# Kernel optimization log

Measured on AMD Instinct MI355X. Metric: run time of the kernel, lower is better.

The kernel has to match this reference:

```python
import jax, jax.numpy as jnp
import numpy as np

B, CIN, H, W = 8, 128, 32, 32
COUT, K, STRIDE, PAD = 128, 3, 1, 1
DK, DV, NH = 64, 64, 8
DKH, DVH = DK // NH, DV // NH


def conv2d(x, w, b, stride, pad):
    out = jax.lax.conv_general_dilated(
        x, w, (stride, stride), [(pad, pad), (pad, pad)],
        dimension_numbers=("NCHW", "OIHW", "NCHW"))
    return out + b[None, :, None, None]


def rel_to_abs(x):
    # x: (b, Nh, L, 2L-1) relative -> (b, Nh, L, L) absolute via pad/reshape/slice
    b, nh, L, _ = x.shape
    x = jnp.pad(x, ((0, 0), (0, 0), (0, 0), (0, 1)))          # (b,Nh,L,2L)
    flat = x.reshape(b, nh, L * 2 * L)
    flat = jnp.pad(flat, ((0, 0), (0, 0), (0, L - 1)))
    final = flat.reshape(b, nh, L + 1, 2 * L - 1)
    return final[:, :, :L, L - 1:]


def relative_logits_1d(q, key_rel, Hh, Ww, Nh, case):
    # q: (b, Nh, x, y, dkh); key_rel: (2*len-1, dkh)
    rel = jnp.einsum("bhxyd,md->bhxym", q, key_rel)
    rel = rel.reshape(-1, Nh * Hh, Ww, 2 * Ww - 1)
    rel = rel_to_abs(rel)
    rel = rel.reshape(-1, Nh, Hh, Ww, Ww)
    rel = jnp.tile(rel[:, :, :, None, :, :], (1, 1, 1, Hh, 1, 1))  # (b,Nh,H,H,W,W)
    if case == "h":
        # torch .transpose(2,4).transpose(3,5)
        rel = rel.transpose(0, 1, 4, 5, 2, 3)
    return rel.reshape(-1, Nh, Hh * Ww, Hh * Ww)


def reference(x, w_general, b_general, w_qkv, b_qkv, w_out, b_out, key_rel_h, key_rel_w):
    batch, _, height, width = x.shape
    conv_out = conv2d(x, w_general, b_general, STRIDE, PAD)

    qkv = conv2d(x, w_qkv, b_qkv, 1, 0)
    q, k, v = jnp.split(qkv, [DK, 2 * DK], axis=1)
    # split heads: (B, Nh, c//Nh, H, W)
    q = q.reshape(batch, NH, DKH, height, width)
    k = k.reshape(batch, NH, DKH, height, width)
    v = v.reshape(batch, NH, DVH, height, width)
    # faithful to original bug: q / dkh**(-0.5) == q * sqrt(dkh)
    q = q / (DKH ** (-0.5))

    flat_q = q.reshape(batch, NH, height * width, DKH)
    flat_k = k.reshape(batch, NH, height * width, DKH)
    flat_v = v.reshape(batch, NH, height * width, DVH)

    logits = jnp.einsum("bhnd,bhmd->bhnm", flat_q, flat_k)

    # relative position logits
    q5 = q.transpose(0, 1, 3, 4, 2)  # (B, Nh, H, W, dkh)
    logits = logits + relative_logits_1d(q5, key_rel_h, height, width, NH, "h")
    logits = logits + relative_logits_1d(q5.transpose(0, 1, 3, 2, 4), key_rel_w, height, width, NH, "w")

    weights = jax.nn.softmax(logits, axis=-1)
    attn = jnp.einsum("bhnm,bhmd->bhnd", weights, flat_v)
    attn = attn.reshape(batch, NH, height, width, DVH)
    # combine heads: (B, Nh*dvh, H, W)
    attn = attn.transpose(0, 1, 4, 2, 3).reshape(batch, NH * DVH, height, width)
    attn = conv2d(attn, w_out, b_out, STRIDE, PAD)
    return jnp.concatenate((conv_out, attn), axis=1)


def setup_inputs():
    key = jax.random.key(0)
    ks = jax.random.split(key, 8)
    f = jnp.float32
    x = jax.random.normal(ks[0], (B, CIN, H, W), f)
    w_general = jax.random.normal(ks[1], (COUT - DV, CIN, K, K), f) * 0.02
    b_general = jnp.zeros((COUT - DV,), f)
    w_qkv = jax.random.normal(ks[2], (2 * DK + DV, CIN, 1, 1), f) * 0.05
    b_qkv = jnp.zeros((2 * DK + DV,), f)
    w_out = jax.random.normal(ks[3], (DV, DV, K, K), f) * 0.05
    b_out = jnp.zeros((DV,), f)
    key_rel_h = jax.random.normal(ks[4], (2 * H - 1, DKH), f)
    key_rel_w = jax.random.normal(ks[5], (2 * W - 1, DKH), f)
    return {"x": x, "w_general": w_general, "b_general": b_general,
            "w_qkv": w_qkv, "b_qkv": b_qkv, "w_out": w_out, "b_out": b_out,
            "key_rel_h": key_rel_h, "key_rel_w": key_rel_w}
```

## Files before the change

### kernel.cpp

```cpp
#include <hip/hip_runtime.h>
#include <hip/hip_bf16.h>


#define NP 1024
#define QSCALE 2.8284271247461903f
#define LOG2E  1.4426950408889634f

using bf16 = __hip_bfloat16;
typedef unsigned short ushort;
typedef unsigned int uint;
using bf16x8 = __attribute__((ext_vector_type(8))) short;
using f32x4  = __attribute__((ext_vector_type(4))) float;
using f32x2  = __attribute__((ext_vector_type(2))) float;

__device__ __forceinline__ float b2f(bf16 v) { return __bfloat162float(v); }
__device__ __forceinline__ ushort f2b(float v) {
  bf16 h = __float2bfloat16(v);
  ushort u; __builtin_memcpy(&u, &h, 2); return u;
}
__device__ __forceinline__ f32x2 up2(uint u) {
  f32x2 r;
  r[0] = __uint_as_float(u << 16);
  r[1] = __uint_as_float(u & 0xffff0000u);
  return r;
}

__device__ __forceinline__ float dot8(const float* a, const float* b) {
  float s = a[0] * b[0];
  s = fmaf(a[1], b[1], s); s = fmaf(a[2], b[2], s); s = fmaf(a[3], b[3], s);
  s = fmaf(a[4], b[4], s); s = fmaf(a[5], b[5], s); s = fmaf(a[6], b[6], s);
  s = fmaf(a[7], b[7], s);
  return s;
}

__device__ __forceinline__ int fenc(float f) { int i = __float_as_int(f); return i < 0 ? (i ^ 0x7fffffff) : i; }
__device__ __forceinline__ float fdec(int i) { return __int_as_float(i < 0 ? (i ^ 0x7fffffff) : i); }

#if defined(__has_builtin)
#if __has_builtin(__builtin_amdgcn_exp2f)
#define EXP2F __builtin_amdgcn_exp2f
#else
#define EXP2F exp2f
#endif
#else
#define EXP2F exp2f
#endif

#define OFF_QBUF   0
#define OFF_KB16   524288
#define OFF_VTB    786432
#define OFF_XPB    1310720
#define OFF_APB    1902592
#define OFF_WGB    2198528
#define OFF_WOB    2235392
#define OFF_BG     2253824
#define OFF_BQKV   2253888
#define OFF_BO     2254080
#define OFF_KRH    2254144
#define OFF_KRW    2254648
#define OFF_FLAG   2255152

__global__ __launch_bounds__(256) void cvt_kernel(
    const void* __restrict__ p0, const void* __restrict__ p1, const void* __restrict__ p2,
    const void* __restrict__ p3, const void* __restrict__ p4, const void* __restrict__ p5,
    const void* __restrict__ p6, const void* __restrict__ p7, const void* __restrict__ p8,
    float* __restrict__ ws, int* __restrict__ flag)
{
  __shared__ int partial[4];
  __shared__ uint lds[64][65];
  int t = threadIdx.x;
  const unsigned* xraw = (const unsigned*)p0;
  int cnt = 0;
  for (int i = t; i < 1024; i += 256) {
    unsigned elo = (xraw[i] >> 7) & 0xffu;
    cnt += (elo >= 64u && elo <= 133u) ? 1 : 0;
  }
#pragma unroll
  for (int off = 1; off < 64; off <<= 1) cnt += __shfl_xor(cnt, off);
  if ((t & 63) == 0) partial[t >> 6] = cnt;
  __syncthreads();
  int tot = partial[0] + partial[1] + partial[2] + partial[3];
  int f32 = (tot >= 650) ? 0 : 1;
  if (blockIdx.x == 0 && t == 0) *flag = f32;

  int gsz = gridDim.x * 256;
  int gid = blockIdx.x * 256 + t;

  const void* src[5] = {p2, p4, p6, p7, p8};
  const int   n[5]    = {64, 192, 64, 504, 504};
  const int   doff[5] = {OFF_BG, OFF_BQKV, OFF_BO, OFF_KRH, OFF_KRW};
#pragma unroll
  for (int s = 0; s < 5; s++) {
    float* dst = ws + doff[s];
    if (f32) { const float* sp = (const float*)src[s];
      for (int i = gid; i < n[s]; i += gsz) dst[i] = sp[i];
    } else { const bf16* sp = (const bf16*)src[s];
      for (int i = gid; i < n[s]; i += gsz) dst[i] = b2f(sp[i]);
    }
  }

  {
    float4* z = (float4*)(ws + OFF_VTB);
    for (int i = gid; i < 131072; i += gsz) z[i] = float4{0.f, 0.f, 0.f, 0.f};
  }

  {
    uint4 z = {0u, 0u, 0u, 0u};
    uint4* xp = (uint4*)(ws + OFF_XPB);
    uint4* ap = (uint4*)(ws + OFF_APB);
    for (int s = gid; s < 9248; s += gsz) {
      int pb = s / 1156, rem = s - pb * 1156;
      int y = rem / 34, x = rem - y * 34;
      if (y == 0 || y == 33 || x == 0 || x == 33) {
        uint4* d1 = xp + (size_t)s * 16;
#pragma unroll
        for (int k = 0; k < 16; k++) d1[k] = z;
        uint4* d2 = ap + (size_t)s * 8;
#pragma unroll
        for (int k = 0; k < 8; k++) d2[k] = z;
      }
    }
  }

  {
    ushort* wgb = (ushort*)(ws + OFF_WGB);
    for (int s = gid; s < 73728; s += gsz) {
      int kykx = s >> 13, co = (s >> 7) & 63, ci = s & 127;
      int si = (co * 128 + ci) * 9 + kykx;
      wgb[s] = f32 ? f2b(((const float*)p1)[si]) : ((const ushort*)p1)[si];
    }
  }
  {
    ushort* wob = (ushort*)(ws + OFF_WOB);
    for (int s = gid; s < 36864; s += gsz) {
      int kykx = s >> 12, co = (s >> 6) & 63, ci = s & 63;
      int si = (co * 64 + ci) * 9 + kykx;
      wob[s] = f32 ? f2b(((const float*)p5)[si]) : ((const ushort*)p5)[si];
    }
  }

  if (blockIdx.x < 128) {
    int w = t >> 6, lane = t & 63;
    int b = blockIdx.x >> 4;
    int pp0 = (blockIdx.x & 15) * 64;
    if (f32) {
      const float* xs = (const float*)p0 + (size_t)b * 131072 + pp0;
#pragma unroll 4
      for (int i = 0; i < 16; i++) {
        int cp = w * 16 + i;
        float v0 = xs[(size_t)(2 * cp) * 1024 + lane];
        float v1 = xs[(size_t)(2 * cp + 1) * 1024 + lane];
        lds[cp][lane] = (uint)f2b(v0) | ((uint)f2b(v1) << 16);
      }
    } else {
      const ushort* xs = (const ushort*)p0 + (size_t)b * 131072 + pp0;
#pragma unroll 4
      for (int i = 0; i < 16; i++) {
        int cp = w * 16 + i;
        uint v0 = xs[(size_t)(2 * cp) * 1024 + lane];
        uint v1 = xs[(size_t)(2 * cp + 1) * 1024 + lane];
        lds[cp][lane] = v0 | (v1 << 16);
      }
    }
    __syncthreads();
    uint* xp32 = (uint*)(ws + OFF_XPB);
#pragma unroll 4
    for (int i = 0; i < 16; i++) {
      int p = w * 16 + i;
      int pp = pp0 + p;
      int y = pp >> 5, x = pp & 31;
      xp32[((size_t)(b * 34 + y + 1) * 34 + x + 1) * 64 + lane] = lds[lane][p];
    }
  }
}

__global__ __launch_bounds__(256) void qkv_kernel(
    const void* __restrict__ xin, const void* __restrict__ wraw, const float* __restrict__ bias,
    float* __restrict__ qbuf, ushort* __restrict__ kb16, ushort* __restrict__ vtb,
    const int* __restrict__ flag)
{
  __shared__ float xt[128][64];
  __shared__ float wt[128][36];
  int b = blockIdx.x, pg = blockIdx.y, cog = blockIdx.z;
  int t = threadIdx.x;
  int p0 = pg * 64;
  int f32 = *flag;
  if (f32) {
    const float* xs = (const float*)xin + (size_t)b * 131072;
    for (int idx = t; idx < 8192; idx += 256) {
      int ci = idx >> 6, p = idx & 63;
      xt[ci][p] = xs[ci * 1024 + p0 + p];
    }
    const float* wsrc = (const float*)wraw;
    for (int idx = t; idx < 4096; idx += 256) {
      int co = idx >> 7, ci = idx & 127;
      wt[ci][co] = wsrc[(cog * 32 + co) * 128 + ci];
    }
  } else {
    const bf16* xs = (const bf16*)xin + (size_t)b * 131072;
    for (int idx = t; idx < 8192; idx += 256) {
      int ci = idx >> 6, p = idx & 63;
      xt[ci][p] = b2f(xs[ci * 1024 + p0 + p]);
    }
    const bf16* wsrc = (const bf16*)wraw;
    for (int idx = t; idx < 4096; idx += 256) {
      int co = idx >> 7, ci = idx & 127;
      wt[ci][co] = b2f(wsrc[(cog * 32 + co) * 128 + ci]);
    }
  }
  __syncthreads();

  int cog2 = t >> 5;
  int pl = (t & 31) * 2;
  float a0[4] = {0.f, 0.f, 0.f, 0.f};
  float a1[4] = {0.f, 0.f, 0.f, 0.f};
  for (int ci = 0; ci < 128; ci++) {
    float2 xv = *(const float2*)&xt[ci][pl];
    float4 wv = *(const float4*)&wt[ci][cog2 * 4];
    a0[0] = fmaf(xv.x, wv.x, a0[0]); a1[0] = fmaf(xv.y, wv.x, a1[0]);
    a0[1] = fmaf(xv.x, wv.y, a0[1]); a1[1] = fmaf(xv.y, wv.y, a1[1]);
    a0[2] = fmaf(xv.x, wv.z, a0[2]); a1[2] = fmaf(xv.y, wv.z, a1[2]);
    a0[3] = fmaf(xv.x, wv.w, a0[3]); a1[3] = fmaf(xv.y, wv.w, a1[3]);
  }

  if (cog < 2) {
#pragma unroll
    for (int j = 0; j < 4; j++) {
      int co = cog * 32 + cog2 * 4 + j;
      float bv = bias[co];
      float2 pk; pk.x = (a0[j] + bv) * QSCALE; pk.y = (a1[j] + bv) * QSCALE;
      *(float2*)(qbuf + ((size_t)b * 64 + co) * NP + p0 + pl) = pk;
    }
  } else if (cog < 4) {
    uint* dstb = (uint*)kb16;
    int chbase = (cog & 1) * 32;
#pragma unroll
    for (int j = 0; j < 4; j++) {
      int co = cog * 32 + cog2 * 4 + j;
      int ch = chbase + cog2 * 4 + j;
      float bv = bias[co];
      uint u = (uint)f2b(a0[j] + bv) | ((uint)f2b(a1[j] + bv) << 16);
      dstb[(((size_t)b * 64 + ch) * NP + p0 + pl) >> 1] = u;
    }
  } else {
    int chbase = (cog & 1) * 32;
    int px = p0 + pl;
#pragma unroll
    for (int j = 0; j < 4; j++) {
      int co = cog * 32 + cog2 * 4 + j;
      int ch = chbase + cog2 * 4 + j;
      float bv = bias[co];
      int h = ch >> 3;
      int d0 = px & 7;
      int m  = (ch & 7) * 128 + (px >> 3);
      ushort* vt = vtb + ((size_t)(b * 8 + h) * 16 + d0) * 1024 + m;
      vt[0]    = f2b(a0[j] + bv);
      vt[1024] = f2b(a1[j] + bv);
    }
  }
}

__global__ __launch_bounds__(256, 4) void attn_kernel(
    const float* __restrict__ qbuf, const ushort* __restrict__ kb16, const ushort* __restrict__ vtb,
    const float* __restrict__ krh, const float* __restrict__ krw,
    ushort* __restrict__ apb)
{
  __shared__ float bw2[2][NP];
  __shared__ float bhT[2][32][32];
  __shared__ float qsT[2][32][8];
  __shared__ float krhs[64][8];
  __shared__ float krws[64][8];
  __shared__ ushort Plds[4][16][40];
  __shared__ float lred[4][16];
  __shared__ int smax[3];

  int t = threadIdx.x;
  int cp = blockIdx.x, h = blockIdx.y, b = blockIdx.z;
  int C0 = cp * 2;
  const float* qbase = qbuf + ((size_t)b * 64 + h * 8) * NP;
  const uint4* kb4 = (const uint4*)(kb16 + ((size_t)b * 64 + h * 8) * NP);
  const ushort* vth = vtb + (size_t)(b * 8 + h) * 16384;

  if (t < 3) smax[t] = (t == 0) ? 0 : fenc(-3.0e38f);

  for (int idx = t; idx < 63 * 8; idx += 256) {
    krhs[idx >> 3][idx & 7] = krh[idx];
    krws[idx >> 3][idx & 7] = krw[idx];
  }
  for (int idx = t; idx < 512; idx += 256) {
    int cs = idx >> 8, d = (idx >> 5) & 7, r = idx & 31;
    qsT[cs][r][d] = qbase[(size_t)d * NP + r * 32 + (C0 + cs)];
  }
  float kn2 = 0.f;
#pragma unroll
  for (int rr = 0; rr < 4; rr++) {
    uint4 ku = kb4[rr * 256 + t];
    f32x2 k0 = up2(ku.x), k1 = up2(ku.y), k2 = up2(ku.z), k3 = up2(ku.w);
    f32x2 s2 = k0 * k0;
    s2 = __builtin_elementwise_fma(k1, k1, s2);
    s2 = __builtin_elementwise_fma(k2, k2, s2);
    s2 = __builtin_elementwise_fma(k3, k3, s2);
    kn2 = fmaxf(kn2, s2[0] + s2[1]);
  }
  __syncthreads();
  atomicMax(&smax[0], __float_as_int(kn2));

  float bwm = -3.0e38f;
  for (int idx = t; idx < 2048; idx += 256) {
    int cs = idx >> 10, m = idx & 1023;
    int rg = m >> 5, j2 = m & 31;
    float s = dot8(qsT[cs][rg], krws[j2 - rg + 31]) * LOG2E;
    bw2[cs][m] = s;
    bwm = fmaxf(bwm, s);
  }
  float bhm = -3.0e38f;
  for (int idx = t; idx < 2048; idx += 256) {
    int cs = idx >> 10, r = idx & 1023;
    int i = r >> 5, J = r & 31;
    float s = dot8(qsT[cs][i], krhs[J - (C0 + cs) + 31]) * LOG2E;
    bhT[cs][i][J] = s;
    bhm = fmaxf(bhm, s);
  }
  atomicMax(&smax[1], fenc(bwm));
  atomicMax(&smax[2], fenc(bhm));
  __syncthreads();

  float kmaxn = sqrtf(__int_as_float(smax[0]));
  float bmax = fdec(smax[1]) + fdec(smax[2]);

  int w = t >> 6, lane = t & 63;
  int quad = lane >> 4, nIdx = lane & 15;
  int n0 = cp * 64 + w * 16;
  int nQ = n0 + nIdx;
  int Cs = w >> 1;
  int J = ((w & 1) << 4) + nIdx;

  const bf16x8 zero8 = {0, 0, 0, 0, 0, 0, 0, 0};

  const float* qrow = qbase + (size_t)nQ * 8;
  bf16x8 Bq = zero8;
  float nn = 0.f;
  ushort ub[8];
#pragma unroll
  for (int d = 0; d < 8; d++) {
    float v = qrow[d] * LOG2E;
    ub[d] = f2b(v);
    float vr = __uint_as_float((uint)ub[d] << 16);
    nn = fmaf(vr, vr, nn);
  }
  if (quad == 0) {
#pragma unroll
    for (int d = 0; d < 8; d++) Bq[d] = (short)ub[d];
  }
  float Mn = sqrtf(nn) * kmaxn + bmax;

  f32x4 accO = {0.f, 0.f, 0.f, 0.f};
  float lpart = 0.f;
  ushort* prow = &Plds[w][nIdx][0];

#pragma unroll 2
  for (int mc = 0; mc < 32; ++mc) {
    int mb = mc * 32;
    float pre = bhT[Cs][mc][J] - Mn;
    ushort pb[8];
#pragma unroll
    for (int s = 0; s < 2; ++s) {
      int mt = mb + s * 16;
      bf16x8 Ak = *(const bf16x8*)(kb4 + mt + nIdx);
      if (quad != 0) Ak = zero8;
      f32x4 S = __builtin_amdgcn_mfma_f32_16x16x32_bf16(Ak, Bq, f32x4{0.f,0.f,0.f,0.f}, 0, 0, 0);
      float4 bw4 = *(const float4*)&bw2[Cs][mt + (quad << 2)];
      const float bwv[4] = {bw4.x, bw4.y, bw4.z, bw4.w};
#pragma unroll
      for (int r = 0; r < 4; ++r) {
        float p = EXP2F(S[r] + bwv[r] + pre);
        lpart += p;
        pb[s * 4 + r] = f2b(p);
      }
    }
    uint2 w0, w1;
    w0.x = (uint)pb[0] | ((uint)pb[1] << 16);
    w0.y = (uint)pb[2] | ((uint)pb[3] << 16);
    w1.x = (uint)pb[4] | ((uint)pb[5] << 16);
    w1.y = (uint)pb[6] | ((uint)pb[7] << 16);
    *(uint2*)(prow + (quad << 2))        = w0;
    *(uint2*)(prow + 16 + (quad << 2))   = w1;
    bf16x8 Ap = *(const bf16x8*)(prow + (quad << 3));
    bf16x8 Bv = *(const bf16x8*)(vth + (size_t)nIdx * 1024 + mb + (quad << 3));
    accO = __builtin_amdgcn_mfma_f32_16x16x32_bf16(Ap, Bv, accO, 0, 0, 0);
  }

  lpart += __shfl_xor(lpart, 16);
  lpart += __shfl_xor(lpart, 32);
  if (lane < 16) lred[w][lane] = lpart;
  float4 lr4 = *(const float4*)&lred[w][quad << 2];
  const float lr[4] = {lr4.x, lr4.y, lr4.z, lr4.w};

  if (nIdx < 8) {
#pragma unroll
    for (int r = 0; r < 4; ++r) {
      int n = n0 + (quad << 2) + r;
      float v = accO[r] / lr[r];
      apb[((size_t)(b * 34 + (n >> 5) + 1) * 34 + (n & 31) + 1) * 64 + h * 8 + nIdx] = f2b(v);
    }
  }
}

template <int CINT>
__global__ __launch_bounds__(256) void conv_mfma_kernel(
    const ushort* __restrict__ xp, const ushort* __restrict__ wp,
    const float* __restrict__ bias, void* __restrict__ out,
    int co_base, const int* __restrict__ flag)
{
  int pt = blockIdx.x;
  int b  = blockIdx.y;
  int lane = threadIdx.x & 63;
  int w = threadIdx.x >> 6;
  int n = lane & 15;
  int kg = lane >> 4;
  int p0 = pt * 16;
  int y = p0 >> 5, x0 = p0 & 31;

  const ushort* abase = wp + (size_t)(w * 16 + n) * CINT + kg * 8;
  const ushort* bbase = xp + ((size_t)(b * 34 + y) * 34 + x0 + n) * CINT + kg * 8;

  f32x4 acc0 = {0.f, 0.f, 0.f, 0.f};
  f32x4 acc1 = {0.f, 0.f, 0.f, 0.f};
#pragma unroll
  for (int c = 0; c < CINT / 32; c++) {
    int ci0 = c * 32;
#pragma unroll
    for (int kp = 0; kp < 9; kp++) {
      int ky = kp / 3, kx = kp - ky * 3;
      bf16x8 A = *(const bf16x8*)(abase + (size_t)kp * 64 * CINT + ci0);
      bf16x8 B = *(const bf16x8*)(bbase + (size_t)(ky * 34 + kx) * CINT + ci0);
      if (kp & 1) acc1 = __builtin_amdgcn_mfma_f32_16x16x32_bf16(A, B, acc1, 0, 0, 0);
      else        acc0 = __builtin_amdgcn_mfma_f32_16x16x32_bf16(A, B, acc0, 0, 0, 0);
    }
  }

  int f32o = *flag;
#pragma unroll
  for (int r = 0; r < 4; r++) {
    int co = w * 16 + kg * 4 + r;
    float v = acc0[r] + acc1[r] + bias[co];
    size_t eoff = ((size_t)b * 128 + co_base + co) * 1024 + p0 + n;
    if (f32o) ((float*)out)[eoff] = v;
    else ((bf16*)out)[eoff] = __float2bfloat16(v);
  }
}

extern "C" void kernel_launch(void* const* d_in, const int* in_sizes, int n_in,
                              void* d_out, int out_size, void* d_ws, size_t ws_size,
                              hipStream_t stream) {
  float* ws = (float*)d_ws;
  float*  qbuf  = ws + OFF_QBUF;
  ushort* kb16  = (ushort*)(ws + OFF_KB16);
  ushort* vtb   = (ushort*)(ws + OFF_VTB);
  ushort* xpb   = (ushort*)(ws + OFF_XPB);
  ushort* apb   = (ushort*)(ws + OFF_APB);
  ushort* wgb   = (ushort*)(ws + OFF_WGB);
  ushort* wob   = (ushort*)(ws + OFF_WOB);
  float*  bgf   = ws + OFF_BG;
  float*  bqkvf = ws + OFF_BQKV;
  float*  bof   = ws + OFF_BO;
  float*  krhf  = ws + OFF_KRH;
  float*  krwf  = ws + OFF_KRW;
  int*    flag  = (int*)(ws + OFF_FLAG);

  cvt_kernel<<<512, 256, 0, stream>>>(d_in[0], d_in[1], d_in[2], d_in[3], d_in[4],
                                      d_in[5], d_in[6], d_in[7], d_in[8], ws, flag);
  qkv_kernel<<<dim3(8, 16, 6), 256, 0, stream>>>(d_in[0], d_in[3], bqkvf, qbuf, kb16, vtb, flag);
  conv_mfma_kernel<128><<<dim3(64, 8), 256, 0, stream>>>(xpb, wgb, bgf, d_out, 0, flag);
  attn_kernel<<<dim3(16, 8, 8), 256, 0, stream>>>(qbuf, kb16, vtb, krhf, krwf, apb);
  conv_mfma_kernel<64><<<dim3(64, 8), 256, 0, stream>>>(apb, wob, bof, d_out, 64, flag);
}
```

Before: 159.0 us.

## Use MFMA for QKV projection and fuse general conv into attention launch

Replaces the scalar FP32 QKV 1x1 conv with an MFMA bf16 kernel that reads the padded NHWC bf16 input produced by the conversion kernel, after converting the QKV weights to bf16 there. It also merges the general 3x3 conv into the attention kernel's grid as extra blocks, so both run concurrently in one launch. The key_rel shared arrays are padded to 12 floats per row. Together these aim to cut QKV compute time and launch/serialization overhead, at the cost of bf16 precision in the projection and attention-kernel resource limits applying to the conv blocks.

```diff
diff --git a/kernel.cpp b/kernel.cpp
--- a/kernel.cpp
+++ b/kernel.cpp
@@ -59,6 +59,7 @@
 #define OFF_KRH    2254144
 #define OFF_KRW    2254648
 #define OFF_FLAG   2255152
+#define OFF_WQB    2255168
 
 __global__ __launch_bounds__(256) void cvt_kernel(
     const void* __restrict__ p0, const void* __restrict__ p1, const void* __restrict__ p2,
@@ -136,6 +137,12 @@
       int kykx = s >> 12, co = (s >> 6) & 63, ci = s & 63;
       int si = (co * 64 + ci) * 9 + kykx;
       wob[s] = f32 ? f2b(((const float*)p5)[si]) : ((const ushort*)p5)[si];
+    }
+  }
+  {
+    ushort* wqb = (ushort*)(ws + OFF_WQB);
+    for (int s = gid; s < 24576; s += gsz) {
+      wqb[s] = f32 ? f2b(((const float*)p3)[s]) : ((const ushort*)p3)[s];
     }
   }
 
@@ -174,108 +181,145 @@
   }
 }
 
-__global__ __launch_bounds__(256) void qkv_kernel(
-    const void* __restrict__ xin, const void* __restrict__ wraw, const float* __restrict__ bias,
-    float* __restrict__ qbuf, ushort* __restrict__ kb16, ushort* __restrict__ vtb,
-    const int* __restrict__ flag)
+__global__ __launch_bounds__(256) void qkv_mfma_kernel(
+    const ushort* __restrict__ xp, const ushort* __restrict__ wqb,
+    const float* __restrict__ bias, float* __restrict__ qbuf,
+    ushort* __restrict__ kb16, ushort* __restrict__ vtb)
 {
-  __shared__ float xt[128][64];
-  __shared__ float wt[128][36];
-  int b = blockIdx.x, pg = blockIdx.y, cog = blockIdx.z;
-  int t = threadIdx.x;
-  int p0 = pg * 64;
-  int f32 = *flag;
-  if (f32) {
-    const float* xs = (const float*)xin + (size_t)b * 131072;
-    for (int idx = t; idx < 8192; idx += 256) {
-      int ci = idx >> 6, p = idx & 63;
-      xt[ci][p] = xs[ci * 1024 + p0 + p];
-    }
-    const float* wsrc = (const float*)wraw;
-    for (int idx = t; idx < 4096; idx += 256) {
-      int co = idx >> 7, ci = idx & 127;
-      wt[ci][co] = wsrc[(cog * 32 + co) * 128 + ci];
-    }
-  } else {
-    const bf16* xs = (const bf16*)xin + (size_t)b * 131072;
-    for (int idx = t; idx < 8192; idx += 256) {
-      int ci = idx >> 6, p = idx & 63;
-      xt[ci][p] = b2f(xs[ci * 1024 + p0 + p]);
-    }
-    const bf16* wsrc = (const bf16*)wraw;
-    for (int idx = t; idx < 4096; idx += 256) {
-      int co = idx >> 7, ci = idx & 127;
-      wt[ci][co] = b2f(wsrc[(cog * 32 + co) * 128 + ci]);
-    }
-  }
-  __syncthreads();
-
-  int cog2 = t >> 5;
-  int pl = (t & 31) * 2;
-  float a0[4] = {0.f, 0.f, 0.f, 0.f};
-  float a1[4] = {0.f, 0.f, 0.f, 0.f};
-  for (int ci = 0; ci < 128; ci++) {
-    float2 xv = *(const float2*)&xt[ci][pl];
-    float4 wv = *(const float4*)&wt[ci][cog2 * 4];
-    a0[0] = fmaf(xv.x, wv.x, a0[0]); a1[0] = fmaf(xv.y, wv.x, a1[0]);
-    a0[1] = fmaf(xv.x, wv.y, a0[1]); a1[1] = fmaf(xv.y, wv.y, a1[1]);
-    a0[2] = fmaf(xv.x, wv.z, a0[2]); a1[2] = fmaf(xv.y, wv.z, a1[2]);
-    a0[3] = fmaf(xv.x, wv.w, a0[3]); a1[3] = fmaf(xv.y, wv.w, a1[3]);
-  }
-
-  if (cog < 2) {
-#pragma unroll
-    for (int j = 0; j < 4; j++) {
-      int co = cog * 32 + cog2 * 4 + j;
-      float bv = bias[co];
-      float2 pk; pk.x = (a0[j] + bv) * QSCALE; pk.y = (a1[j] + bv) * QSCALE;
-      *(float2*)(qbuf + ((size_t)b * 64 + co) * NP + p0 + pl) = pk;
-    }
-  } else if (cog < 4) {
-    uint* dstb = (uint*)kb16;
-    int chbase = (cog & 1) * 32;
-#pragma unroll
-    for (int j = 0; j < 4; j++) {
-      int co = cog * 32 + cog2 * 4 + j;
-      int ch = chbase + cog2 * 4 + j;
-      float bv = bias[co];
-      uint u = (uint)f2b(a0[j] + bv) | ((uint)f2b(a1[j] + bv) << 16);
-      dstb[(((size_t)b * 64 + ch) * NP + p0 + pl) >> 1] = u;
-    }
-  } else {
-    int chbase = (cog & 1) * 32;
-    int px = p0 + pl;
-#pragma unroll
-    for (int j = 0; j < 4; j++) {
-      int co = cog * 32 + cog2 * 4 + j;
-      int ch = chbase + cog2 * 4 + j;
-      float bv = bias[co];
-      int h = ch >> 3;
-      int d0 = px & 7;
-      int m  = (ch & 7) * 128 + (px >> 3);
-      ushort* vt = vtb + ((size_t)(b * 8 + h) * 16 + d0) * 1024 + m;
-      vt[0]    = f2b(a0[j] + bv);
-      vt[1024] = f2b(a1[j] + bv);
-    }
-  }
-}
-
-__global__ __launch_bounds__(256, 4) void attn_kernel(
+  int pt = blockIdx.x;
+  int b  = blockIdx.y;
+  int lane = threadIdx.x & 63;
+  int w = threadIdx.x >> 6;
+  int n = lane & 15;
+  int kg = lane >> 4;
+  int p0 = pt * 16;
+  int px = p0 + n;
+  int y = px >> 5, x = px & 31;
+
+  const ushort* bbase = xp + ((size_t)(b * 34 + y + 1) * 34 + (x + 1)) * 128 + kg * 8;
+  bf16x8 Bf[4];
+#pragma unroll
+  for (int c = 0; c < 4; c++) Bf[c] = *(const bf16x8*)(bbase + c * 32);
+
+  f32x4 acc0 = {0.f, 0.f, 0.f, 0.f};
+  f32x4 acc1 = {0.f, 0.f, 0.f, 0.f};
+  f32x4 acc2 = {0.f, 0.f, 0.f, 0.f};
+  {
+    const ushort* abase = wqb + (size_t)(w * 16 + n) * 128 + kg * 8;
+#pragma unroll
+    for (int c = 0; c < 4; c++) {
+      bf16x8 A = *(const bf16x8*)(abase + c * 32);
+      acc0 = __builtin_amdgcn_mfma_f32_16x16x32_bf16(A, Bf[c], acc0, 0, 0, 0);
+    }
+  }
+  {
+    const ushort* abase = wqb + (size_t)((w + 4) * 16 + n) * 128 + kg * 8;
+#pragma unroll
+    for (int c = 0; c < 4; c++) {
+      bf16x8 A = *(const bf16x8*)(abase + c * 32);
+      acc1 = __builtin_amdgcn_mfma_f32_16x16x32_bf16(A, Bf[c], acc1, 0, 0, 0);
+    }
+  }
+  {
+    const ushort* abase = wqb + (size_t)((w + 8) * 16 + n) * 128 + kg * 8;
+#pragma unroll
+    for (int c = 0; c < 4; c++) {
+      bf16x8 A = *(const bf16x8*)(abase + c * 32);
+      acc2 = __builtin_amdgcn_mfma_f32_16x16x32_bf16(A, Bf[c], acc2, 0, 0, 0);
+    }
+  }
+
+#pragma unroll
+  for (int r = 0; r < 4; r++) {
+    int co = w * 16 + kg * 4 + r;
+    float v = acc0[r] + bias[co];
+    qbuf[((size_t)b * 64 + co) * NP + px] = v * QSCALE;
+  }
+#pragma unroll
+  for (int r = 0; r < 4; r++) {
+    int co = (w + 4) * 16 + kg * 4 + r;
+    float v = acc1[r] + bias[co];
+    kb16[((size_t)b * 64 + (co - 64)) * NP + px] = f2b(v);
+  }
+#pragma unroll
+  for (int r = 0; r < 4; r++) {
+    int co = (w + 8) * 16 + kg * 4 + r;
+    float v = acc2[r] + bias[co];
+    int ch = co - 128;
+    int h = ch >> 3;
+    int d0 = px & 7;
+    int m  = (ch & 7) * 128 + (px >> 3);
+    vtb[((size_t)(b * 8 + h) * 16 + d0) * 1024 + m] = f2b(v);
+  }
+}
+
+template <int CINT>
+__device__ __forceinline__ void conv_body(
+    const ushort* __restrict__ xp, const ushort* __restrict__ wp,
+    const float* __restrict__ bias, void* __restrict__ out,
+    int co_base, const int* __restrict__ flag, int pt, int b)
+{
+  int lane = threadIdx.x & 63;
+  int w = threadIdx.x >> 6;
+  int n = lane & 15;
+  int kg = lane >> 4;
+  int p0 = pt * 16;
+  int y = p0 >> 5, x0 = p0 & 31;
+
+  const ushort* abase = wp + (size_t)(w * 16 + n) * CINT + kg * 8;
+  const ushort* bbase = xp + ((size_t)(b * 34 + y) * 34 + x0 + n) * CINT + kg * 8;
+
+  f32x4 acc0 = {0.f, 0.f, 0.f, 0.f};
+  f32x4 acc1 = {0.f, 0.f, 0.f, 0.f};
+#pragma unroll
+  for (int c = 0; c < CINT / 32; c++) {
+    int ci0 = c * 32;
+#pragma unroll
+    for (int kp = 0; kp < 9; kp++) {
+      int ky = kp / 3, kx = kp - ky * 3;
+      bf16x8 A = *(const bf16x8*)(abase + (size_t)kp * 64 * CINT + ci0);
+      bf16x8 B = *(const bf16x8*)(bbase + (size_t)(ky * 34 + kx) * CINT + ci0);
+      if (kp & 1) acc1 = __builtin_amdgcn_mfma_f32_16x16x32_bf16(A, B, acc1, 0, 0, 0);
+      else        acc0 = __builtin_amdgcn_mfma_f32_16x16x32_bf16(A, B, acc0, 0, 0, 0);
+    }
+  }
+
+  int f32o = *flag;
+#pragma unroll
+  for (int r = 0; r < 4; r++) {
+    int co = w * 16 + kg * 4 + r;
+    float v = acc0[r] + acc1[r] + bias[co];
+    size_t eoff = ((size_t)b * 128 + co_base + co) * 1024 + p0 + n;
+    if (f32o) ((float*)out)[eoff] = v;
+    else ((bf16*)out)[eoff] = __float2bfloat16(v);
+  }
+}
+
+__global__ __launch_bounds__(256, 4) void attn_conv_kernel(
     const float* __restrict__ qbuf, const ushort* __restrict__ kb16, const ushort* __restrict__ vtb,
     const float* __restrict__ krh, const float* __restrict__ krw,
-    ushort* __restrict__ apb)
+    ushort* __restrict__ apb,
+    const ushort* __restrict__ xp, const ushort* __restrict__ wgb,
+    const float* __restrict__ bg, void* __restrict__ out, const int* __restrict__ flag)
 {
+  int bx = blockIdx.x;
+  if (bx >= 1024) {
+    int id = bx - 1024;
+    conv_body<128>(xp, wgb, bg, out, 0, flag, id & 63, id >> 6);
+    return;
+  }
+
   __shared__ float bw2[2][NP];
   __shared__ float bhT[2][32][32];
   __shared__ float qsT[2][32][8];
-  __shared__ float krhs[64][8];
-  __shared__ float krws[64][8];
+  __shared__ __align__(16) float krhs[64][12];
+  __shared__ __align__(16) float krws[64][12];
   __shared__ ushort Plds[4][16][40];
   __shared__ float lred[4][16];
   __shared__ int smax[3];
 
   int t = threadIdx.x;
-  int cp = blockIdx.x, h = blockIdx.y, b = blockIdx.z;
+  int cp = bx & 15, h = (bx >> 4) & 7, b = bx >> 7;
   int C0 = cp * 2;
   const float* qbase = qbuf + ((size_t)b * 64 + h * 8) * NP;
   const uint4* kb4 = (const uint4*)(kb16 + ((size_t)b * 64 + h * 8) * NP);
@@ -412,42 +456,7 @@
     const float* __restrict__ bias, void* __restrict__ out,
     int co_base, const int* __restrict__ flag)
 {
-  int pt = blockIdx.x;
-  int b  = blockIdx.y;
-  int lane = threadIdx.x & 63;
-  int w = threadIdx.x >> 6;
-  int n = lane & 15;
-  int kg = lane >> 4;
-  int p0 = pt * 16;
-  int y = p0 >> 5, x0 = p0 & 31;
-
-  const ushort* abase = wp + (size_t)(w * 16 + n) * CINT + kg * 8;
-  const ushort* bbase = xp + ((size_t)(b * 34 + y) * 34 + x0 + n) * CINT + kg * 8;
-
-  f32x4 acc0 = {0.f, 0.f, 0.f, 0.f};
-  f32x4 acc1 = {0.f, 0.f, 0.f, 0.f};
-#pragma unroll
-  for (int c = 0; c < CINT / 32; c++) {
-    int ci0 = c * 32;
-#pragma unroll
-    for (int kp = 0; kp < 9; kp++) {
-      int ky = kp / 3, kx = kp - ky * 3;
-      bf16x8 A = *(const bf16x8*)(abase + (size_t)kp * 64 * CINT + ci0);
-      bf16x8 B = *(const bf16x8*)(bbase + (size_t)(ky * 34 + kx) * CINT + ci0);
-      if (kp & 1) acc1 = __builtin_amdgcn_mfma_f32_16x16x32_bf16(A, B, acc1, 0, 0, 0);
-      else        acc0 = __builtin_amdgcn_mfma_f32_16x16x32_bf16(A, B, acc0, 0, 0, 0);
-    }
-  }
-
-  int f32o = *flag;
-#pragma unroll
-  for (int r = 0; r < 4; r++) {
-    int co = w * 16 + kg * 4 + r;
-    float v = acc0[r] + acc1[r] + bias[co];
-    size_t eoff = ((size_t)b * 128 + co_base + co) * 1024 + p0 + n;
-    if (f32o) ((float*)out)[eoff] = v;
-    else ((bf16*)out)[eoff] = __float2bfloat16(v);
-  }
+  conv_body<CINT>(xp, wp, bias, out, co_base, flag, blockIdx.x, blockIdx.y);
 }
 
 extern "C" void kernel_launch(void* const* d_in, const int* in_sizes, int n_in,
@@ -461,6 +470,7 @@
   ushort* apb   = (ushort*)(ws + OFF_APB);
   ushort* wgb   = (ushort*)(ws + OFF_WGB);
   ushort* wob   = (ushort*)(ws + OFF_WOB);
+  ushort* wqb   = (ushort*)(ws + OFF_WQB);
   float*  bgf   = ws + OFF_BG;
   float*  bqkvf = ws + OFF_BQKV;
   float*  bof   = ws + OFF_BO;
@@ -470,8 +480,8 @@
 
   cvt_kernel<<<512, 256, 0, stream>>>(d_in[0], d_in[1], d_in[2], d_in[3], d_in[4],
                                       d_in[5], d_in[6], d_in[7], d_in[8], ws, flag);
-  qkv_kernel<<<dim3(8, 16, 6), 256, 0, stream>>>(d_in[0], d_in[3], bqkvf, qbuf, kb16, vtb, flag);
-  conv_mfma_kernel<128><<<dim3(64, 8), 256, 0, stream>>>(xpb, wgb, bgf, d_out, 0, flag);
-  attn_kernel<<<dim3(16, 8, 8), 256, 0, stream>>>(qbuf, kb16, vtb, krhf, krwf, apb);
+  qkv_mfma_kernel<<<dim3(64, 8), 256, 0, stream>>>(xpb, wqb, bqkvf, qbuf, kb16, vtb);
+  attn_conv_kernel<<<1536, 256, 0, stream>>>(qbuf, kb16, vtb, krhf, krwf, apb,
+                                             xpb, wgb, bgf, d_out, flag);
   conv_mfma_kernel<64><<<dim3(64, 8), 256, 0, stream>>>(apb, wob, bof, d_out, 64, flag);
 }
```

After: 142.7 us. 1.11x faster.
